# Kernel optimization log

Measured on AMD Instinct MI355X. Metric: run time of the kernel, lower is better.

## Reference

```python
import jax, jax.numpy as jnp
import numpy as np

N, H, W = 128, 400, 400          # instances, feature canvas
MS = 28                          # mask_size = pooler_resolution*2
CT, CS = 80, 53                  # thing / stuff classes
STRIDE = 4                       # common_stride
HG, WG = 1600, 1600              # image-resolution gt panoptic
IGNORE = 255
LOSS_W = 1.0


def setup_inputs() -> dict:
    key = jax.random.key(0)
    ks = jax.random.split(key, 8)
    mask_logits = jax.random.normal(ks[0], (N, CT, MS, MS), jnp.float32)
    stuff_logit = jax.random.normal(ks[1], (CS, H, W), jnp.float32)
    thing_logit = jax.random.normal(ks[2], (CT, H, W), jnp.float32)
    # valid boxes in image pixel coords (x0,y0,x2,y2), width/height >= 16 px
    x0 = jax.random.uniform(ks[3], (N,), minval=0.0, maxval=1200.0)
    y0 = jax.random.uniform(ks[4], (N,), minval=0.0, maxval=1200.0)
    wh = jax.random.uniform(ks[5], (N, 2), minval=16.0, maxval=400.0)
    x2 = jnp.minimum(x0 + wh[:, 0], WG - 1.0)
    y2 = jnp.minimum(y0 + wh[:, 1], HG - 1.0)
    bbox = jnp.stack([x0, y0, x2, y2], axis=1).astype(jnp.float32)
    cls_idx = jax.random.randint(ks[6], (N,), 0, CT, dtype=jnp.int32)
    gt_panoptic = jax.random.randint(ks[7], (HG, WG), 0, CS + N, dtype=jnp.int32)
    return {"mask_logits": mask_logits, "stuff_logit": stuff_logit,
            "thing_logit": thing_logit, "bbox": bbox, "cls_idx": cls_idx,
            "gt_panoptic": gt_panoptic}


def _axis_sample(lo, size, grid, src_size):
    """Bilinear sampling coords along one axis (align_corners=False).
    lo: [N] box start (feat px, int); size: [N] box extent; grid: [G].
    Returns (idx0, idx1, frac) each [N, G]."""
    dst = grid[None, :].astype(jnp.float32) - lo[:, None].astype(jnp.float32)
    src = (dst + 0.5) * (src_size / size[:, None].astype(jnp.float32)) - 0.5
    f = jnp.floor(src)
    t = src - f
    i0 = jnp.clip(f, 0, src_size - 1).astype(jnp.int32)
    i1 = jnp.clip(f + 1, 0, src_size - 1).astype(jnp.int32)
    return i0, i1, t


def reference(mask_logits, stuff_logit, thing_logit, bbox, cls_idx, gt_panoptic):
    # _separate_fetch_logits: gather per-instance class channel -> [N, MS, MS]
    ml = mask_logits[jnp.arange(N), cls_idx]

    # _unmap_mask_logit_single: boxes -> feat coords (.long() == floor, boxes >= 0)
    bl = jnp.floor(bbox / STRIDE).astype(jnp.int32)
    x0b, y0b, x2b, y2b = bl[:, 0], bl[:, 1], bl[:, 2], bl[:, 3]
    hh = y2b - y0b + 1
    ww = x2b - x0b + 1
    ys = jnp.arange(H, dtype=jnp.int32)
    xs = jnp.arange(W, dtype=jnp.int32)

    i0, i1, ty = _axis_sample(y0b, hh, ys, MS)   # [N, H]
    j0, j1, tx = _axis_sample(x0b, ww, xs, MS)   # [N, W]

    # separable bilinear: rows [N, H, MS] then cols [N, H, W]
    r0 = jnp.take_along_axis(ml, jnp.broadcast_to(i0[:, :, None], (N, H, MS)), axis=1)
    r1 = jnp.take_along_axis(ml, jnp.broadcast_to(i1[:, :, None], (N, H, MS)), axis=1)
    rows = r0 * (1.0 - ty)[:, :, None] + r1 * ty[:, :, None]
    c0 = jnp.take_along_axis(rows, jnp.broadcast_to(j0[:, None, :], (N, H, W)), axis=2)
    c1 = jnp.take_along_axis(rows, jnp.broadcast_to(j1[:, None, :], (N, H, W)), axis=2)
    val = c0 * (1.0 - tx)[:, None, :] + c1 * tx[:, None, :]

    vy = (ys[None, :] >= jnp.maximum(y0b, 0)[:, None]) & (ys[None, :] <= jnp.minimum(y2b, H - 1)[:, None])
    vx = (xs[None, :] >= jnp.maximum(x0b, 0)[:, None]) & (xs[None, :] <= jnp.minimum(x2b, W - 1)[:, None])
    thing_mask_logit = jnp.where(vy[:, :, None] & vx[:, None, :], val, 0.0)

    # _crop_thing_logit_single: int()/round() based crop window
    bf = bbox / STRIDE
    cx1 = bf[:, 0].astype(jnp.int32)
    cy1 = bf[:, 1].astype(jnp.int32)
    cx2 = (jnp.round(bf[:, 2]) + 1.0).astype(jnp.int32)
    cy2 = (jnp.round(bf[:, 3]) + 1.0).astype(jnp.int32)
    my = (ys[None, :] >= cy1[:, None]) & (ys[None, :] < cy2[:, None])
    mx = (xs[None, :] >= cx1[:, None]) & (xs[None, :] < cx2[:, None])
    thing_sem_logit = jnp.where(my[:, :, None] & mx[:, None, :], thing_logit[cls_idx], 0.0)

    pan_logit = jnp.concatenate(
        [stuff_logit[None], (thing_mask_logit + thing_sem_logit)[None]], axis=1)

    # gt nearest-downsample to feat_size, then CE with ignore_index
    iy = jnp.floor(jnp.arange(H) * (HG / H)).astype(jnp.int32)
    ix = jnp.floor(jnp.arange(W) * (WG / W)).astype(jnp.int32)
    gt_ds = gt_panoptic[iy[:, None], ix[None, :]][None]          # [1, H, W]
    logp = jax.nn.log_softmax(pan_logit, axis=1)
    tgt = jnp.clip(gt_ds, 0, CS + N - 1)
    nll = -jnp.take_along_axis(logp, tgt[:, None], axis=1)[:, 0]  # [1, H, W]
    valid = gt_ds != IGNORE
    pan_loss = LOSS_W * jnp.sum(jnp.where(valid, nll, 0.0)) / jnp.maximum(
        jnp.sum(valid).astype(jnp.float32), 1.0)
    return pan_logit, pan_loss
```

## Files before the change

### kernel.cpp

```cpp
#include <hip/hip_runtime.h>
#include <math.h>

#define N_   128
#define H_   400
#define W_   400
#define MS_  28
#define CT_  80
#define CS_  53
#define HW_  (H_*W_)
#define NCH_ (CS_ + N_)
#define WG_  1600
#define IGN_ 255
#define G_   8
#define CPG_ 23
#define PPT_ 4
#define BT_  256
#define PPB_ (BT_*PPT_)
#define GX_  ((HW_ + PPB_ - 1)/PPB_)

typedef float f4 __attribute__((ext_vector_type(4)));

struct NParam {
  int vy_lo, vy_hi, vx_lo, vx_hi;
  int cy1, cy2, cx1, cx2;
  float sy, sx;
  int y0b, x0b;
  int mlbase, thbase;
  int pad0, pad1;
};

__device__ float        g_acc[2];
__device__ unsigned int g_done;
__device__ float        g_lp[G_*HW_];
__device__ float        g_vt[HW_];

__device__ __forceinline__ void lse_update(float v, float& m, float& s) {
  float d = v - m;
  float e = __expf(-fabsf(d));
  s = (d > 0.0f) ? fmaf(s, e, 1.0f) : (s + e);
  m = fmaxf(m, v);
}

__global__ __launch_bounds__(256) void main_kernel(
    const float* __restrict__ mask_logits,
    const float* __restrict__ stuff_logit,
    const float* __restrict__ thing_logit,
    const float* __restrict__ bbox,
    const int*   __restrict__ cls_idx,
    const int*   __restrict__ gt,
    float* __restrict__ out)
{
  __shared__ NParam spar[N_];
  __shared__ int4   sbox[N_];
  int tid = threadIdx.x;
  if (blockIdx.x == 0 && blockIdx.y == 0 && tid == 0) {
    g_acc[0] = 0.0f; g_acc[1] = 0.0f; g_done = 0u;
  }
  if (tid < N_) {
    int n = tid;
    float b0 = bbox[4*n+0]*0.25f, b1 = bbox[4*n+1]*0.25f,
          b2 = bbox[4*n+2]*0.25f, b3 = bbox[4*n+3]*0.25f;
    int x0b = (int)floorf(b0), y0b = (int)floorf(b1);
    int x2b = (int)floorf(b2), y2b = (int)floorf(b3);
    int hh = y2b - y0b + 1, ww = x2b - x0b + 1;
    NParam p;
    p.vy_lo = max(y0b, 0); p.vy_hi = min(y2b, H_-1);
    p.vx_lo = max(x0b, 0); p.vx_hi = min(x2b, W_-1);
    p.cy1 = (int)b1; p.cx1 = (int)b0;
    p.cy2 = (int)(rintf(b3) + 1.0f);
    p.cx2 = (int)(rintf(b2) + 1.0f);
    p.sy = 28.0f / (float)hh; p.sx = 28.0f / (float)ww;
    p.y0b = y0b; p.x0b = x0b;
    int cls = cls_idx[n];
    p.mlbase = (n*CT_ + cls)*(MS_*MS_);
    p.thbase = cls*HW_;
    p.pad0 = 0; p.pad1 = 0;
    spar[n] = p;
    sbox[n] = make_int4(min(p.vy_lo, p.cy1), max(p.vy_hi, p.cy2 - 1),
                        min(p.vx_lo, p.cx1), max(p.vx_hi, p.cx2 - 1));
  }
  __syncthreads();

  int pix0 = (blockIdx.x*BT_ + tid)*PPT_;
  if (pix0 >= HW_) return;
  int y  = pix0 / W_;
  int xb = pix0 - y*W_;

  int grp = blockIdx.y;
  int c0 = grp*CPG_;
  int c1 = min(NCH_, c0 + CPG_);

  int tcs[PPT_];
  #pragma unroll
  for (int k = 0; k < PPT_; ++k) {
    int g = gt[y*(4*WG_) + (xb + k)*4];
    tcs[k] = min(max(g, 0), NCH_-1);
  }

  float mv[PPT_], sv[PPT_], vts[PPT_];
  #pragma unroll
  for (int k = 0; k < PPT_; ++k) { mv[k] = -INFINITY; sv[k] = 0.0f; vts[k] = 0.0f; }
  int zc = 0;

  int c = c0;
  for (; c < min(c1, CS_); ++c) {
    f4 v = *(const f4*)(stuff_logit + c*HW_ + pix0);
    *(f4*)(out + c*HW_ + pix0) = v;
    #pragma unroll
    for (int k = 0; k < PPT_; ++k) {
      lse_update(v[k], mv[k], sv[k]);
      if (c == tcs[k]) vts[k] = v[k];
    }
  }
  for (; c < c1; ++c) {
    int n = c - CS_;
    int4 u = sbox[n];
    bool rej = (y < u.x) | (y > u.y) | (xb > u.w) | (xb + PPT_ - 1 < u.z);
    if (__all(rej)) {
      f4 z = {0.0f, 0.0f, 0.0f, 0.0f};
      *(f4*)(out + c*HW_ + pix0) = z;
      ++zc;
      continue;
    }
    NParam p = spar[n];
    float vv[PPT_] = {0.0f, 0.0f, 0.0f, 0.0f};
    if (y >= p.cy1 && y < p.cy2 && xb < p.cx2 && xb+PPT_-1 >= p.cx1) {
      f4 t = *(const f4*)(thing_logit + p.thbase + pix0);
      #pragma unroll
      for (int k = 0; k < PPT_; ++k) {
        int x = xb + k;
        if (x >= p.cx1 && x < p.cx2) vv[k] = t[k];
      }
    }
    if (y >= p.vy_lo && y <= p.vy_hi && xb <= p.vx_hi && xb+PPT_-1 >= p.vx_lo) {
      float srcy = ((float)(y - p.y0b) + 0.5f)*p.sy - 0.5f;
      float fy = floorf(srcy); float ty = srcy - fy;
      int i0 = (int)fminf(fmaxf(fy,        0.0f), (float)(MS_-1));
      int i1 = (int)fminf(fmaxf(fy + 1.0f, 0.0f), (float)(MS_-1));
      const float* r0p = mask_logits + p.mlbase + i0*MS_;
      const float* r1p = mask_logits + p.mlbase + i1*MS_;
      #pragma unroll
      for (int k = 0; k < PPT_; ++k) {
        int x = xb + k;
        if (x >= p.vx_lo && x <= p.vx_hi) {
          float srcx = ((float)(x - p.x0b) + 0.5f)*p.sx - 0.5f;
          float fx = floorf(srcx); float tx = srcx - fx;
          int j0 = (int)fminf(fmaxf(fx,        0.0f), (float)(MS_-1));
          int j1 = (int)fminf(fmaxf(fx + 1.0f, 0.0f), (float)(MS_-1));
          float r0 = r0p[j0]*(1.0f - tx) + r0p[j1]*tx;
          float r1 = r1p[j0]*(1.0f - tx) + r1p[j1]*tx;
          vv[k] += r0*(1.0f - ty) + r1*ty;
        }
      }
    }
    f4 ov = {vv[0], vv[1], vv[2], vv[3]};
    *(f4*)(out + c*HW_ + pix0) = ov;
    #pragma unroll
    for (int k = 0; k < PPT_; ++k) {
      lse_update(vv[k], mv[k], sv[k]);
      if (c == tcs[k]) vts[k] = vv[k];
    }
  }

  float zcf = (float)zc;
  f4 lp;
  #pragma unroll
  for (int k = 0; k < PPT_; ++k) {
    float m = mv[k], s = sv[k];
    if (zc > 0) {
      if (m >= 0.0f) { s = fmaf(zcf, __expf(-m), s); }
      else           { s = fmaf(s, __expf(m), zcf); m = 0.0f; }
    }
    lp[k] = m + __logf(s);
  }
  *(f4*)(g_lp + grp*HW_ + pix0) = lp;

  #pragma unroll
  for (int k = 0; k < PPT_; ++k)
    if (tcs[k] >= c0 && tcs[k] < c1) g_vt[pix0 + k] = vts[k];
}

__global__ __launch_bounds__(256) void reduce_kernel(
    const int* __restrict__ gt,
    float* __restrict__ out)
{
  int tid = threadIdx.x;
  int pix0 = (blockIdx.x*BT_ + tid)*PPT_;
  float nll = 0.0f, cnt = 0.0f;
  if (pix0 < HW_) {
    f4 l0 = *(const f4*)(g_lp + pix0);
    float mv[PPT_] = {l0.x, l0.y, l0.z, l0.w};
    float sv[PPT_] = {1.0f, 1.0f, 1.0f, 1.0f};
    #pragma unroll
    for (int g = 1; g < G_; ++g) {
      f4 lg4 = *(const f4*)(g_lp + g*HW_ + pix0);
      float lg[PPT_] = {lg4.x, lg4.y, lg4.z, lg4.w};
      #pragma unroll
      for (int k = 0; k < PPT_; ++k) {
        float d = lg[k] - mv[k];
        float e = __expf(-fabsf(d));
        sv[k] = (d > 0.0f) ? fmaf(sv[k], e, 1.0f) : (sv[k] + e);
        mv[k] = fmaxf(mv[k], lg[k]);
      }
    }
    f4 vt4 = *(const f4*)(g_vt + pix0);
    float vt[PPT_] = {vt4.x, vt4.y, vt4.z, vt4.w};
    int y  = pix0 / W_;
    int xb = pix0 - y*W_;
    #pragma unroll
    for (int k = 0; k < PPT_; ++k) {
      int g = gt[y*(4*WG_) + (xb + k)*4];
      bool valid = (g != IGN_);
      nll += valid ? (mv[k] + __logf(sv[k]) - vt[k]) : 0.0f;
      cnt += valid ? 1.0f : 0.0f;
    }
  }

  for (int off = 32; off >= 1; off >>= 1) {
    nll += __shfl_down(nll, off, 64);
    cnt += __shfl_down(cnt, off, 64);
  }
  __shared__ float red[8];
  int lane = tid & 63, wid = tid >> 6;
  if (lane == 0) { red[wid*2] = nll; red[wid*2+1] = cnt; }
  __syncthreads();
  if (tid == 0) {
    float ts  = red[0] + red[2] + red[4] + red[6];
    float tcn = red[1] + red[3] + red[5] + red[7];
    atomicAdd(&g_acc[0], ts);
    atomicAdd(&g_acc[1], tcn);
    __threadfence();
    unsigned int d = atomicAdd(&g_done, 1u);
    if (d == gridDim.x - 1) {
      __threadfence();
      float loss = g_acc[0] / fmaxf(g_acc[1], 1.0f);
      out[NCH_*HW_] = loss;
    }
  }
}

extern "C" void kernel_launch(void* const* d_in, const int* in_sizes, int n_in,
                              void* d_out, int out_size, void* d_ws, size_t ws_size,
                              hipStream_t stream) {
  const float* mask_logits = (const float*)d_in[0];
  const float* stuff_logit = (const float*)d_in[1];
  const float* thing_logit = (const float*)d_in[2];
  const float* bbox        = (const float*)d_in[3];
  const int*   cls_idx     = (const int*)d_in[4];
  const int*   gt          = (const int*)d_in[5];
  float* out = (float*)d_out;

  dim3 grid1(GX_, G_);
  main_kernel<<<grid1, BT_, 0, stream>>>(mask_logits, stuff_logit, thing_logit,
                                         bbox, cls_idx, gt, out);
  reduce_kernel<<<GX_, BT_, 0, stream>>>(gt, out);
}
```

Baseline: 224.5 us.

## Fuse reduction into main kernel via per-tile last-arriver counters

Removes the separate reduce kernel launch. Each pixel tile keeps a counter, and the last of its 8 channel-group blocks to arrive combines the partial log-sum-exps and computes the partial NLL. A global counter then lets the last tile sum the per-block partials deterministically instead of using float atomics. This saves one launch and the inter-kernel gap, at the cost of relaxed-atomic synchronisation that relies on modulo counters never being reset between calls.

```diff
diff --git a/kernel.cpp b/kernel.cpp
--- a/kernel.cpp
+++ b/kernel.cpp
@@ -19,6 +19,7 @@
 #define GX_  ((HW_ + PPB_ - 1)/PPB_)
 
 typedef float f4 __attribute__((ext_vector_type(4)));
+typedef unsigned long long u64;
 
 struct NParam {
   int vy_lo, vy_hi, vx_lo, vx_hi;
@@ -29,10 +30,20 @@
   int pad0, pad1;
 };
 
-__device__ float        g_acc[2];
+__device__ unsigned int g_tdone[GX_];
 __device__ unsigned int g_done;
-__device__ float        g_lp[G_*HW_];
+__device__ u64          g_lp2[(G_*HW_)/2];
 __device__ float        g_vt[HW_];
+__device__ float        g_part[GX_*2];
+
+static __device__ __forceinline__ u64 pack2(float a, float b) {
+  union { float f[2]; u64 u; } t; t.f[0] = a; t.f[1] = b; return t.u;
+}
+static __device__ __forceinline__ void unpack2(u64 u, float& a, float& b) {
+  union { float f[2]; u64 u; } t; t.u = u; a = t.f[0]; b = t.f[1];
+}
+#define AG_ST(p, v) __hip_atomic_store((p), (v), __ATOMIC_RELAXED, __HIP_MEMORY_SCOPE_AGENT)
+#define AG_LD(p)    __hip_atomic_load((p), __ATOMIC_RELAXED, __HIP_MEMORY_SCOPE_AGENT)
 
 __device__ __forceinline__ void lse_update(float v, float& m, float& s) {
   float d = v - m;
@@ -52,10 +63,9 @@
 {
   __shared__ NParam spar[N_];
   __shared__ int4   sbox[N_];
+  __shared__ float  red[8];
+  __shared__ unsigned s_tick, s_fin;
   int tid = threadIdx.x;
-  if (blockIdx.x == 0 && blockIdx.y == 0 && tid == 0) {
-    g_acc[0] = 0.0f; g_acc[1] = 0.0f; g_done = 0u;
-  }
   if (tid < N_) {
     int n = tid;
     float b0 = bbox[4*n+0]*0.25f, b1 = bbox[4*n+1]*0.25f,
@@ -82,136 +92,149 @@
   __syncthreads();
 
   int pix0 = (blockIdx.x*BT_ + tid)*PPT_;
-  if (pix0 >= HW_) return;
-  int y  = pix0 / W_;
-  int xb = pix0 - y*W_;
-
+  bool act = (pix0 < HW_);
   int grp = blockIdx.y;
   int c0 = grp*CPG_;
   int c1 = min(NCH_, c0 + CPG_);
 
-  int tcs[PPT_];
+  int y = 0, xb = 0;
+  int graw[PPT_];
   #pragma unroll
-  for (int k = 0; k < PPT_; ++k) {
-    int g = gt[y*(4*WG_) + (xb + k)*4];
-    tcs[k] = min(max(g, 0), NCH_-1);
-  }
-
-  float mv[PPT_], sv[PPT_], vts[PPT_];
-  #pragma unroll
-  for (int k = 0; k < PPT_; ++k) { mv[k] = -INFINITY; sv[k] = 0.0f; vts[k] = 0.0f; }
-  int zc = 0;
-
-  int c = c0;
-  for (; c < min(c1, CS_); ++c) {
-    f4 v = *(const f4*)(stuff_logit + c*HW_ + pix0);
-    *(f4*)(out + c*HW_ + pix0) = v;
-    #pragma unroll
-    for (int k = 0; k < PPT_; ++k) {
-      lse_update(v[k], mv[k], sv[k]);
-      if (c == tcs[k]) vts[k] = v[k];
-    }
-  }
-  for (; c < c1; ++c) {
-    int n = c - CS_;
-    int4 u = sbox[n];
-    bool rej = (y < u.x) | (y > u.y) | (xb > u.w) | (xb + PPT_ - 1 < u.z);
-    if (__all(rej)) {
-      f4 z = {0.0f, 0.0f, 0.0f, 0.0f};
-      *(f4*)(out + c*HW_ + pix0) = z;
-      ++zc;
-      continue;
-    }
-    NParam p = spar[n];
-    float vv[PPT_] = {0.0f, 0.0f, 0.0f, 0.0f};
-    if (y >= p.cy1 && y < p.cy2 && xb < p.cx2 && xb+PPT_-1 >= p.cx1) {
-      f4 t = *(const f4*)(thing_logit + p.thbase + pix0);
-      #pragma unroll
-      for (int k = 0; k < PPT_; ++k) {
-        int x = xb + k;
-        if (x >= p.cx1 && x < p.cx2) vv[k] = t[k];
-      }
-    }
-    if (y >= p.vy_lo && y <= p.vy_hi && xb <= p.vx_hi && xb+PPT_-1 >= p.vx_lo) {
-      float srcy = ((float)(y - p.y0b) + 0.5f)*p.sy - 0.5f;
-      float fy = floorf(srcy); float ty = srcy - fy;
-      int i0 = (int)fminf(fmaxf(fy,        0.0f), (float)(MS_-1));
-      int i1 = (int)fminf(fmaxf(fy + 1.0f, 0.0f), (float)(MS_-1));
-      const float* r0p = mask_logits + p.mlbase + i0*MS_;
-      const float* r1p = mask_logits + p.mlbase + i1*MS_;
-      #pragma unroll
-      for (int k = 0; k < PPT_; ++k) {
-        int x = xb + k;
-        if (x >= p.vx_lo && x <= p.vx_hi) {
-          float srcx = ((float)(x - p.x0b) + 0.5f)*p.sx - 0.5f;
-          float fx = floorf(srcx); float tx = srcx - fx;
-          int j0 = (int)fminf(fmaxf(fx,        0.0f), (float)(MS_-1));
-          int j1 = (int)fminf(fmaxf(fx + 1.0f, 0.0f), (float)(MS_-1));
-          float r0 = r0p[j0]*(1.0f - tx) + r0p[j1]*tx;
-          float r1 = r1p[j0]*(1.0f - tx) + r1p[j1]*tx;
-          vv[k] += r0*(1.0f - ty) + r1*ty;
-        }
-      }
-    }
-    f4 ov = {vv[0], vv[1], vv[2], vv[3]};
-    *(f4*)(out + c*HW_ + pix0) = ov;
-    #pragma unroll
-    for (int k = 0; k < PPT_; ++k) {
-      lse_update(vv[k], mv[k], sv[k]);
-      if (c == tcs[k]) vts[k] = vv[k];
-    }
-  }
-
-  float zcf = (float)zc;
-  f4 lp;
-  #pragma unroll
-  for (int k = 0; k < PPT_; ++k) {
-    float m = mv[k], s = sv[k];
-    if (zc > 0) {
-      if (m >= 0.0f) { s = fmaf(zcf, __expf(-m), s); }
-      else           { s = fmaf(s, __expf(m), zcf); m = 0.0f; }
-    }
-    lp[k] = m + __logf(s);
-  }
-  *(f4*)(g_lp + grp*HW_ + pix0) = lp;
-
-  #pragma unroll
-  for (int k = 0; k < PPT_; ++k)
-    if (tcs[k] >= c0 && tcs[k] < c1) g_vt[pix0 + k] = vts[k];
-}
-
-__global__ __launch_bounds__(256) void reduce_kernel(
-    const int* __restrict__ gt,
-    float* __restrict__ out)
-{
-  int tid = threadIdx.x;
-  int pix0 = (blockIdx.x*BT_ + tid)*PPT_;
-  float nll = 0.0f, cnt = 0.0f;
-  if (pix0 < HW_) {
-    f4 l0 = *(const f4*)(g_lp + pix0);
-    float mv[PPT_] = {l0.x, l0.y, l0.z, l0.w};
-    float sv[PPT_] = {1.0f, 1.0f, 1.0f, 1.0f};
-    #pragma unroll
-    for (int g = 1; g < G_; ++g) {
-      f4 lg4 = *(const f4*)(g_lp + g*HW_ + pix0);
-      float lg[PPT_] = {lg4.x, lg4.y, lg4.z, lg4.w};
-      #pragma unroll
-      for (int k = 0; k < PPT_; ++k) {
-        float d = lg[k] - mv[k];
-        float e = __expf(-fabsf(d));
-        sv[k] = (d > 0.0f) ? fmaf(sv[k], e, 1.0f) : (sv[k] + e);
-        mv[k] = fmaxf(mv[k], lg[k]);
-      }
-    }
-    f4 vt4 = *(const f4*)(g_vt + pix0);
-    float vt[PPT_] = {vt4.x, vt4.y, vt4.z, vt4.w};
-    int y  = pix0 / W_;
-    int xb = pix0 - y*W_;
+  for (int k = 0; k < PPT_; ++k) graw[k] = IGN_;
+
+  if (act) {
+    y  = pix0 / W_;
+    xb = pix0 - y*W_;
+
+    int tcs[PPT_];
     #pragma unroll
     for (int k = 0; k < PPT_; ++k) {
       int g = gt[y*(4*WG_) + (xb + k)*4];
-      bool valid = (g != IGN_);
-      nll += valid ? (mv[k] + __logf(sv[k]) - vt[k]) : 0.0f;
+      graw[k] = g;
+      tcs[k] = min(max(g, 0), NCH_-1);
+    }
+
+    float mv[PPT_], sv[PPT_], vts[PPT_];
+    #pragma unroll
+    for (int k = 0; k < PPT_; ++k) { mv[k] = -INFINITY; sv[k] = 0.0f; vts[k] = 0.0f; }
+    int zc = 0;
+
+    int c = c0;
+    for (; c < min(c1, CS_); ++c) {
+      f4 v = *(const f4*)(stuff_logit + c*HW_ + pix0);
+      *(f4*)(out + c*HW_ + pix0) = v;
+      #pragma unroll
+      for (int k = 0; k < PPT_; ++k) {
+        lse_update(v[k], mv[k], sv[k]);
+        if (c == tcs[k]) vts[k] = v[k];
+      }
+    }
+    for (; c < c1; ++c) {
+      int n = c - CS_;
+      int4 u = sbox[n];
+      bool rej = (y < u.x) | (y > u.y) | (xb > u.w) | (xb + PPT_ - 1 < u.z);
+      if (__all(rej)) {
+        f4 z = {0.0f, 0.0f, 0.0f, 0.0f};
+        *(f4*)(out + c*HW_ + pix0) = z;
+        ++zc;
+        continue;
+      }
+      NParam p = spar[n];
+      float vv[PPT_] = {0.0f, 0.0f, 0.0f, 0.0f};
+      if (y >= p.cy1 && y < p.cy2 && xb < p.cx2 && xb+PPT_-1 >= p.cx1) {
+        f4 t = *(const f4*)(thing_logit + p.thbase + pix0);
+        #pragma unroll
+        for (int k = 0; k < PPT_; ++k) {
+          int x = xb + k;
+          if (x >= p.cx1 && x < p.cx2) vv[k] = t[k];
+        }
+      }
+      if (y >= p.vy_lo && y <= p.vy_hi && xb <= p.vx_hi && xb+PPT_-1 >= p.vx_lo) {
+        float srcy = ((float)(y - p.y0b) + 0.5f)*p.sy - 0.5f;
+        float fy = floorf(srcy); float ty = srcy - fy;
+        int i0 = (int)fminf(fmaxf(fy,        0.0f), (float)(MS_-1));
+        int i1 = (int)fminf(fmaxf(fy + 1.0f, 0.0f), (float)(MS_-1));
+        const float* r0p = mask_logits + p.mlbase + i0*MS_;
+        const float* r1p = mask_logits + p.mlbase + i1*MS_;
+        #pragma unroll
+        for (int k = 0; k < PPT_; ++k) {
+          int x = xb + k;
+          if (x >= p.vx_lo && x <= p.vx_hi) {
+            float srcx = ((float)(x - p.x0b) + 0.5f)*p.sx - 0.5f;
+            float fx = floorf(srcx); float tx = srcx - fx;
+            int j0 = (int)fminf(fmaxf(fx,        0.0f), (float)(MS_-1));
+            int j1 = (int)fminf(fmaxf(fx + 1.0f, 0.0f), (float)(MS_-1));
+            float r0 = r0p[j0]*(1.0f - tx) + r0p[j1]*tx;
+            float r1 = r1p[j0]*(1.0f - tx) + r1p[j1]*tx;
+            vv[k] += r0*(1.0f - ty) + r1*ty;
+          }
+        }
+      }
+      f4 ov = {vv[0], vv[1], vv[2], vv[3]};
+      *(f4*)(out + c*HW_ + pix0) = ov;
+      #pragma unroll
+      for (int k = 0; k < PPT_; ++k) {
+        lse_update(vv[k], mv[k], sv[k]);
+        if (c == tcs[k]) vts[k] = vv[k];
+      }
+    }
+
+    float zcf = (float)zc;
+    float lpv[PPT_];
+    #pragma unroll
+    for (int k = 0; k < PPT_; ++k) {
+      float m = mv[k], s = sv[k];
+      if (zc > 0) {
+        if (m >= 0.0f) { s = fmaf(zcf, __expf(-m), s); }
+        else           { s = fmaf(s, __expf(m), zcf); m = 0.0f; }
+      }
+      lpv[k] = m + __logf(s);
+    }
+    int base = (grp*HW_ + pix0) >> 1;
+    AG_ST(&g_lp2[base],     pack2(lpv[0], lpv[1]));
+    AG_ST(&g_lp2[base + 1], pack2(lpv[2], lpv[3]));
+    #pragma unroll
+    for (int k = 0; k < PPT_; ++k)
+      if (tcs[k] >= c0 && tcs[k] < c1) AG_ST(&g_vt[pix0 + k], vts[k]);
+  }
+
+  __syncthreads();
+  if (tid == 0)
+    s_tick = __hip_atomic_fetch_add(&g_tdone[blockIdx.x], 1u,
+                                    __ATOMIC_RELAXED, __HIP_MEMORY_SCOPE_AGENT);
+  __syncthreads();
+  if ((s_tick & (unsigned)(G_-1)) != (unsigned)(G_-1)) return;
+
+  float nll = 0.0f, cnt = 0.0f;
+  if (act) {
+    float m2[PPT_], s2[PPT_];
+    {
+      u64 a = AG_LD(&g_lp2[pix0 >> 1]);
+      u64 b = AG_LD(&g_lp2[(pix0 >> 1) + 1]);
+      unpack2(a, m2[0], m2[1]); unpack2(b, m2[2], m2[3]);
+      #pragma unroll
+      for (int k = 0; k < PPT_; ++k) s2[k] = 1.0f;
+    }
+    #pragma unroll
+    for (int g = 1; g < G_; ++g) {
+      int base = (g*HW_ + pix0) >> 1;
+      u64 a = AG_LD(&g_lp2[base]);
+      u64 b = AG_LD(&g_lp2[base + 1]);
+      float lg[PPT_];
+      unpack2(a, lg[0], lg[1]); unpack2(b, lg[2], lg[3]);
+      #pragma unroll
+      for (int k = 0; k < PPT_; ++k) {
+        float d = lg[k] - m2[k];
+        float e = __expf(-fabsf(d));
+        s2[k] = (d > 0.0f) ? fmaf(s2[k], e, 1.0f) : (s2[k] + e);
+        m2[k] = fmaxf(m2[k], lg[k]);
+      }
+    }
+    #pragma unroll
+    for (int k = 0; k < PPT_; ++k) {
+      float vt = AG_LD(&g_vt[pix0 + k]);
+      bool valid = (graw[k] != IGN_);
+      nll += valid ? (m2[k] + __logf(s2[k]) - vt) : 0.0f;
       cnt += valid ? 1.0f : 0.0f;
     }
   }
@@ -220,21 +243,36 @@
     nll += __shfl_down(nll, off, 64);
     cnt += __shfl_down(cnt, off, 64);
   }
-  __shared__ float red[8];
   int lane = tid & 63, wid = tid >> 6;
   if (lane == 0) { red[wid*2] = nll; red[wid*2+1] = cnt; }
   __syncthreads();
   if (tid == 0) {
     float ts  = red[0] + red[2] + red[4] + red[6];
     float tcn = red[1] + red[3] + red[5] + red[7];
-    atomicAdd(&g_acc[0], ts);
-    atomicAdd(&g_acc[1], tcn);
-    __threadfence();
-    unsigned int d = atomicAdd(&g_done, 1u);
-    if (d == gridDim.x - 1) {
-      __threadfence();
-      float loss = g_acc[0] / fmaxf(g_acc[1], 1.0f);
-      out[NCH_*HW_] = loss;
+    AG_ST(&g_part[blockIdx.x*2],     ts);
+    AG_ST(&g_part[blockIdx.x*2 + 1], tcn);
+    asm volatile("s_waitcnt vmcnt(0)" ::: "memory");
+    unsigned d = __hip_atomic_fetch_add(&g_done, 1u,
+                                        __ATOMIC_RELAXED, __HIP_MEMORY_SCOPE_AGENT);
+    s_fin = ((d % (unsigned)GX_) == (unsigned)(GX_-1)) ? 1u : 0u;
+  }
+  __syncthreads();
+  if (s_fin) {
+    float a = 0.0f, b = 0.0f;
+    if (tid < GX_) {
+      a = AG_LD(&g_part[tid*2]);
+      b = AG_LD(&g_part[tid*2 + 1]);
+    }
+    for (int off = 32; off >= 1; off >>= 1) {
+      a += __shfl_down(a, off, 64);
+      b += __shfl_down(b, off, 64);
+    }
+    if (lane == 0) { red[wid*2] = a; red[wid*2+1] = b; }
+    __syncthreads();
+    if (tid == 0) {
+      float ts  = red[0] + red[2] + red[4] + red[6];
+      float tcn = red[1] + red[3] + red[5] + red[7];
+      out[NCH_*HW_] = ts / fmaxf(tcn, 1.0f);
     }
   }
 }
@@ -253,5 +291,4 @@
   dim3 grid1(GX_, G_);
   main_kernel<<<grid1, BT_, 0, stream>>>(mask_logits, stuff_logit, thing_logit,
                                          bbox, cls_idx, gt, out);
-  reduce_kernel<<<GX_, BT_, 0, stream>>>(gt, out);
-}
+}
```

Result: no change. 220.2 us (-1.9%).
